# Performance work log

Hardware: AMD Instinct MI355X
Metric: run time of the kernel (lower is better)

Reference implementation:

```python
import jax, jax.numpy as jnp
import numpy as np

NORM_EPS = 1e-6
QK_SCALE = 1.0 / 128.0  # 1/d_head (muP)
ROTARY_BASE = 10000
INFTY_APPROX = 1e30

B, T, M, H, D = 2, 2048, 1024, 8, 128


def _rmsnorm(x, eps=NORM_EPS):
    # normalize over the last (head) dim; no learned gains (norm_gains=False)
    ms = jnp.mean(jnp.square(x), axis=-1, keepdims=True)
    return x / jnp.sqrt(ms + eps)


def _rope(x, base=ROTARY_BASE):
    # x: [b, h, t, d]; rotate (even-half, odd-half) pairs as in the source
    length, width = x.shape[-2], x.shape[-1]
    half = width // 2
    pos = jnp.arange(length, dtype=x.dtype)[:, None]            # [t, 1]
    freqs = jnp.power(jnp.asarray(base, x.dtype), -jnp.arange(half, dtype=x.dtype) / half)[None, :]
    rad = pos * freqs                                            # [t, half]
    cos = jnp.cos(rad)[None, None]
    sin = jnp.sin(rad)[None, None]
    even, odd = jnp.split(x, 2, axis=-1)
    return jnp.concatenate([even * cos - odd * sin, even * sin + odd * cos], axis=-1)


def setup_inputs() -> dict:
    key = jax.random.key(0)
    ks = jax.random.split(key, 5)
    std = M ** -0.5
    return {
        "x": jax.random.normal(ks[0], (B, T, M), jnp.float32),
        "wq": jax.random.normal(ks[1], (M, H, D), jnp.float32) * std,
        "wk": jax.random.normal(ks[2], (M, H, D), jnp.float32) * std,
        "wv": jax.random.normal(ks[3], (M, H, D), jnp.float32) * std,
        "wo": jax.random.normal(ks[4], (H, D, M), jnp.float32) * std,
    }


def reference(x, wq, wk, wv, wo):
    # projections: [b, h, t, d]
    q = jnp.einsum('bim,mhd->bhid', x, wq)
    k = jnp.einsum('bim,mhd->bhid', x, wk)
    v = jnp.einsum('bim,mhd->bhid', x, wv)
    # qk RMSNorm (norm_gains=False)
    q = _rmsnorm(q)
    k = _rmsnorm(k)
    # inline RoPE
    q = _rope(q)
    k = _rope(k)
    # scaled scores: mult applied to both q and k (mult^2 = qk_scale)
    mult = jnp.asarray(QK_SCALE ** 0.5, q.dtype)
    s = jnp.einsum('bhid,bhjd->bhij', q * mult, k * mult)
    # causal mask: subtract large constant where i < j
    t = s.shape[-1]
    mask = (jnp.arange(t)[:, None] < jnp.arange(t)[None, :]).astype(s.dtype)
    s = s - jnp.asarray(INFTY_APPROX, s.dtype) * mask[None, None]
    p = jax.nn.softmax(s, axis=-1)
    o = jnp.einsum('bhij,bhjd->bhid', p, v)
    return jnp.einsum('bhid,hdm->bim', o, wo)
```

## Files before the change

kernel.cpp:

```cpp
#include <hip/hip_runtime.h>
#include <hip/hip_bf16.h>
#include <math.h>

#define B_  2
#define T_  2048
#define M_  1024
#define H_  8
#define D_  128
#define NROW (B_ * T_)
#define HD  (H_ * D_)

#define NORM_EPS 1e-6f
#define QK_MULT  0.08838834764831845f
#define LN_BASE_64 0.14391156510f

typedef short bf16x8  __attribute__((ext_vector_type(8)));
typedef float f32x4   __attribute__((ext_vector_type(4)));
typedef float f32x16  __attribute__((ext_vector_type(16)));

static __device__ __forceinline__ unsigned short f2bf(float f) {
    union { __hip_bfloat16 h; unsigned short u; } cv;
    cv.h = __float2bfloat16(f);
    return cv.u;
}
static __device__ __forceinline__ float bf2f(unsigned short u) {
    union { unsigned short u; __hip_bfloat16 h; } cv;
    cv.u = u;
    return __bfloat162float(cv.h);
}
static __device__ __forceinline__ unsigned int pk2bf(float a, float b) {
    return ((unsigned int)f2bf(b) << 16) | f2bf(a);
}

static __device__ __forceinline__ void gload_lds16(const unsigned short* g,
                                                   unsigned short* l) {
    __builtin_amdgcn_global_load_lds(
        (const __attribute__((address_space(1))) void*)g,
        (__attribute__((address_space(3))) void*)l, 16, 0, 0);
}

__global__ __launch_bounds__(256) void prep(const float* __restrict__ x,
                                            const float* __restrict__ w0,
                                            const float* __restrict__ w1,
                                            const float* __restrict__ w2,
                                            const float* __restrict__ w3,
                                            unsigned short* __restrict__ xb,
                                            unsigned short* __restrict__ wqkvT,
                                            unsigned short* __restrict__ woT)
{
    __shared__ float t[32][33];
    const int z = blockIdx.z;
    if (z == 4) {
        const size_t base = ((size_t)blockIdx.y * 32 + blockIdx.x) * 4096;
        #pragma unroll
        for (int it = 0; it < 4; ++it) {
            const size_t i = base + it * 1024 + threadIdx.x * 4;
            const float4 v = *(const float4*)(x + i);
            ushort4 o;
            o.x = f2bf(v.x); o.y = f2bf(v.y); o.z = f2bf(v.z); o.w = f2bf(v.w);
            *(ushort4*)(xb + i) = o;
        }
        return;
    }
    const float* in = z == 0 ? w0 : (z == 1 ? w1 : (z == 2 ? w2 : w3));
    unsigned short* out = z < 3 ? (wqkvT + (size_t)z * 1024 * 1024) : woT;

    const int tx = threadIdx.x & 31;
    const int ty = threadIdx.x >> 5;
    const int n0 = blockIdx.x * 32;
    const int k0 = blockIdx.y * 32;
    #pragma unroll
    for (int r = 0; r < 4; ++r)
        t[ty + r * 8][tx] = in[(size_t)(k0 + ty + r * 8) * 1024 + n0 + tx];
    __syncthreads();
    #pragma unroll
    for (int r = 0; r < 4; ++r)
        out[(size_t)(n0 + ty + r * 8) * 1024 + k0 + tx] = f2bf(t[tx][ty + r * 8]);
}

template <int MODE>
__global__ __launch_bounds__(256) void gemm_bt(const unsigned short* __restrict__ A,
                                               const unsigned short* __restrict__ Bt,
                                               unsigned short* __restrict__ oq,
                                               unsigned short* __restrict__ ok,
                                               unsigned short* __restrict__ vt,
                                               float* __restrict__ cf)
{
    __shared__ __align__(16) unsigned short pool[128 * 132 + 512];
    unsigned short* As = pool;
    unsigned short* Bs = pool + 128 * 32;

    const int tid  = threadIdx.x;
    const int lane = tid & 63;
    const int w    = tid >> 6;
    const int g    = lane >> 4;
    const int lc   = lane & 15;
    const int wm   = w >> 1;
    const int wn   = w & 1;

    const int m0 = blockIdx.y * 128;
    const int n0 = blockIdx.x * 128;

    const unsigned short* aBase = A  + (size_t)m0 * 1024;
    const unsigned short* bBase = Bt + (size_t)n0 * 1024;

    f32x4 acc[4][4];
    #pragma unroll
    for (int i = 0; i < 4; ++i)
        #pragma unroll
        for (int j = 0; j < 4; ++j)
            acc[i][j] = (f32x4){0.f, 0.f, 0.f, 0.f};

    for (int kt = 0; kt < 32; ++kt) {
        const int k0 = kt * 32;
        #pragma unroll
        for (int it = 0; it < 2; ++it) {
            const int u  = tid + it * 256;
            const int r2 = u >> 2;
            const int s2 = u & 3;
            gload_lds16(aBase + (size_t)r2 * 1024 + k0 + s2 * 8, &As[u * 8]);
            gload_lds16(bBase + (size_t)r2 * 1024 + k0 + s2 * 8, &Bs[u * 8]);
        }
        __syncthreads();

        bf16x8 af[4], bfr[4];
        #pragma unroll
        for (int i = 0; i < 4; ++i)
            af[i] = *(const bf16x8*)&As[(wm * 64 + i * 16 + lc) * 32 + g * 8];
        #pragma unroll
        for (int j = 0; j < 4; ++j)
            bfr[j] = *(const bf16x8*)&Bs[(wn * 64 + j * 16 + lc) * 32 + g * 8];

        #pragma unroll
        for (int i = 0; i < 4; ++i)
            #pragma unroll
            for (int j = 0; j < 4; ++j)
                acc[i][j] = __builtin_amdgcn_mfma_f32_16x16x32_bf16(af[i], bfr[j], acc[i][j], 0, 0, 0);
        __syncthreads();
    }

    if (MODE == 0) {
        const int which = n0 >> 10;
        const int ncol0 = (n0 & 1023) + wn * 64;
        if (which < 2) {
            unsigned short* outp = which == 0 ? oq : ok;
            unsigned short* xbuf = pool;
            float* sqbuf = (float*)(pool + 128 * 132);

            float sq[4][4];
            #pragma unroll
            for (int i = 0; i < 4; ++i)
                #pragma unroll
                for (int r = 0; r < 4; ++r) {
                    float s = acc[i][0][r] * acc[i][0][r] + acc[i][1][r] * acc[i][1][r]
                            + acc[i][2][r] * acc[i][2][r] + acc[i][3][r] * acc[i][3][r];
                    #pragma unroll
                    for (int off = 1; off < 16; off <<= 1) s += __shfl_xor(s, off);
                    sq[i][r] = s;
                }
            if (lc == 0) {
                #pragma unroll
                for (int i = 0; i < 4; ++i)
                    #pragma unroll
                    for (int r = 0; r < 4; ++r)
                        sqbuf[wn * 128 + wm * 64 + i * 16 + g * 4 + r] = sq[i][r];
            }
            __syncthreads();

            #pragma unroll
            for (int i = 0; i < 4; ++i)
                #pragma unroll
                for (int r = 0; r < 4; ++r) {
                    const int row = wm * 64 + i * 16 + g * 4 + r;
                    const float tot = sqbuf[row] + sqbuf[128 + row];
                    const float rms = rsqrtf(tot * (1.0f / 128.0f) + NORM_EPS) * QK_MULT;
                    #pragma unroll
                    for (int j = 0; j < 4; ++j) {
                        acc[i][j][r] *= rms;
                        xbuf[row * 132 + wn * 64 + j * 16 + lc] = f2bf(acc[i][j][r]);
                    }
                }
            __syncthreads();

            float freq[4];
            #pragma unroll
            for (int j = 0; j < 4; ++j)
                freq[j] = __expf(-(float)(j * 16 + lc) * LN_BASE_64);
            #pragma unroll
            for (int i = 0; i < 4; ++i)
                #pragma unroll
                for (int r = 0; r < 4; ++r) {
                    const int row  = wm * 64 + i * 16 + g * 4 + r;
                    const int trow = m0 + row;
                    const float tpos = (float)(trow & (T_ - 1));
                    #pragma unroll
                    for (int j = 0; j < 4; ++j) {
                        float sn, cs;
                        __sincosf(tpos * freq[j], &sn, &cs);
                        const float own = acc[i][j][r];
                        const float par = bf2f(xbuf[row * 132 + ((wn ^ 1) * 64) + j * 16 + lc]);
                        const float outv = (wn == 0) ? (own * cs - par * sn)
                                                     : (par * sn + own * cs);
                        outp[(size_t)trow * 1024 + ncol0 + j * 16 + lc] = f2bf(outv);
                    }
                }
        } else {
            const int b2 = m0 >> 11;
            #pragma unroll
            for (int i = 0; i < 4; ++i) {
                const int t = (m0 & 2047) + wm * 64 + i * 16 + g * 4;
                #pragma unroll
                for (int j = 0; j < 4; ++j) {
                    const int nc = ncol0 + j * 16 + lc;
                    const int hh = nc >> 7, dd = nc & 127;
                    uint2 val;
                    val.x = pk2bf(acc[i][j][0], acc[i][j][1]);
                    val.y = pk2bf(acc[i][j][2], acc[i][j][3]);
                    *(uint2*)(vt + (((size_t)(b2 * 8 + hh) * 128 + dd) * T_ + t)) = val;
                }
            }
        }
    } else {
        #pragma unroll
        for (int i = 0; i < 4; ++i) {
            const int mrow = m0 + wm * 64 + i * 16 + g * 4;
            #pragma unroll
            for (int j = 0; j < 4; ++j) {
                const int nc = n0 + wn * 64 + j * 16 + lc;
                #pragma unroll
                for (int r = 0; r < 4; ++r)
                    cf[(size_t)(mrow + r) * 1024 + nc] = acc[i][j][r];
            }
        }
    }
}

__global__ __launch_bounds__(256) void flash_attn(const unsigned short* __restrict__ qb,
                                                  const unsigned short* __restrict__ kb,
                                                  const unsigned short* __restrict__ vt,
                                                  unsigned short* __restrict__ o)
{
    __shared__ __align__(16) unsigned short smem[2 * 64 * 128 + 2 * 128 * 64 + 128];
    unsigned short* KsB = smem;
    unsigned short* VsB = smem + 2 * 64 * 128;
    float* lscr = (float*)(smem + 2 * 64 * 128 + 2 * 128 * 64);
    float* scr  = (float*)smem;

    const int tid  = threadIdx.x;
    const int lane = tid & 63;
    const int w    = tid >> 6;
    const int wj   = w >> 1;
    const int wq2  = w & 1;
    const int qcol = lane & 31;
    const int hi   = lane >> 5;

    const int bh = blockIdx.x;
    const int h  = bh & (H_ - 1);
    const int b  = bh >> 3;
    const int yy = blockIdx.y;
    const int qt = (yy & 1) ? (31 - (yy >> 1)) : (yy >> 1);
    const int q0 = qt * 64;

    const size_t bhbase  = (size_t)b * T_ * HD + (size_t)h * 128;
    const size_t bhvbase = (size_t)bh * 128 * T_;

    int mI[4];
    size_t srcKoff[4], srcVoff[4];
    #pragma unroll
    for (int it = 0; it < 4; ++it) {
        const int m = (w * 4 + it) * 64 + lane;
        mI[it] = m;
        const int jK = m >> 4, cK = (m & 15) ^ (jK & 15);
        srcKoff[it] = (size_t)jK * 1024 + cK * 8;
        const int dV = m >> 3, cV = (m & 7) ^ (dV & 7);
        srcVoff[it] = (size_t)dV * T_ + cV * 8;
    }
    const unsigned short* kgb = kb + bhbase;
    const unsigned short* vgb = vt + bhvbase;

    bf16x8 qf[8];
    {
        const unsigned short* qp = qb + bhbase + (size_t)(q0 + wq2 * 32 + qcol) * 1024 + hi * 8;
        #pragma unroll
        for (int ks = 0; ks < 8; ++ks)
            qf[ks] = *(const bf16x8*)(qp + ks * 16);
    }

    float lsum = 0.f;
    f32x16 otacc[4];
    #pragma unroll
    for (int dch = 0; dch < 4; ++dch)
        #pragma unroll
        for (int r = 0; r < 16; ++r) otacc[dch][r] = 0.f;

    #pragma unroll
    for (int it = 0; it < 4; ++it) {
        gload_lds16(kgb + srcKoff[it], &KsB[mI[it] * 8]);
        gload_lds16(vgb + srcVoff[it], &VsB[mI[it] * 8]);
    }

    for (int jt = 0; jt <= qt; ++jt) {
        const int cur = jt & 1;
        unsigned short* Ks = KsB + cur * (64 * 128);
        unsigned short* Vs = VsB + cur * (128 * 64);
        __syncthreads();

        if (jt < qt) {
            const size_t j0n = (size_t)(jt + 1) * 64;
            unsigned short* Kn = KsB + (cur ^ 1) * (64 * 128);
            unsigned short* Vn = VsB + (cur ^ 1) * (128 * 64);
            #pragma unroll
            for (int it = 0; it < 4; ++it) {
                gload_lds16(kgb + j0n * 1024 + srcKoff[it], &Kn[mI[it] * 8]);
                gload_lds16(vgb + j0n + srcVoff[it], &Vn[mI[it] * 8]);
            }
        }

        const bool dead = (jt == qt) && (wj > wq2);
        if (!dead) {
            f32x16 sacc;
            #pragma unroll
            for (int r = 0; r < 16; ++r) sacc[r] = 0.f;
            const int jrow = wj * 32 + qcol;
            #pragma unroll
            for (int ks = 0; ks < 8; ++ks) {
                const int c = ks * 2 + hi;
                bf16x8 af = *(const bf16x8*)&Ks[(jrow * 16 + (c ^ (lane & 15))) * 8];
                sacc = __builtin_amdgcn_mfma_f32_32x32x16_bf16(af, qf[ks], sacc, 0, 0, 0);
            }

            if (jt == qt && wj == wq2) {
                #pragma unroll
                for (int r = 0; r < 16; ++r) {
                    const int jl = (r & 3) + 8 * (r >> 2) + 4 * hi;
                    if (qcol < jl) sacc[r] = -1e30f;
                }
            }

            unsigned int dw[8];
            #pragma unroll
            for (int m2 = 0; m2 < 8; ++m2) {
                const float p0 = __expf(sacc[2 * m2]);
                const float p1 = __expf(sacc[2 * m2 + 1]);
                lsum += p0 + p1;
                dw[m2] = pk2bf(p0, p1);
            }
            unsigned int ex[8];
            #pragma unroll
            for (int m2 = 0; m2 < 8; ++m2)
                ex[m2] = (unsigned int)__shfl_xor((int)dw[m2], 32);

            #pragma unroll
            for (int ks2 = 0; ks2 < 2; ++ks2) {
                union { unsigned int u[4]; bf16x8 v; } pf;
                pf.u[0] = hi ? ex[4 * ks2 + 2] : dw[4 * ks2 + 0];
                pf.u[1] = hi ? ex[4 * ks2 + 3] : dw[4 * ks2 + 1];
                pf.u[2] = hi ? dw[4 * ks2 + 2] : ex[4 * ks2 + 0];
                pf.u[3] = hi ? dw[4 * ks2 + 3] : ex[4 * ks2 + 1];
                #pragma unroll
                for (int dch = 0; dch < 4; ++dch) {
                    const int c = wj * 4 + ks2 * 2 + hi;
                    const int drow = dch * 32 + qcol;
                    bf16x8 af = *(const bf16x8*)&Vs[(drow * 8 + (c ^ (lane & 7))) * 8];
                    otacc[dch] = __builtin_amdgcn_mfma_f32_32x32x16_bf16(af, pf.v, otacc[dch], 0, 0, 0);
                }
            }
        }
    }

    lsum += __shfl_xor(lsum, 32);
    __syncthreads();

    if (wj == 1) {
        float* s0 = scr + (size_t)(wq2 * 32 + qcol) * 129;
        #pragma unroll
        for (int dch = 0; dch < 4; ++dch)
            #pragma unroll
            for (int r = 0; r < 16; ++r)
                s0[dch * 32 + (r & 3) + 8 * (r >> 2) + 4 * hi] = otacc[dch][r];
        if (hi == 0) lscr[wq2 * 32 + qcol] = lsum;
    }
    __syncthreads();
    if (wj == 0) {
        const float l = lsum + lscr[wq2 * 32 + qcol];
        const float inv = 1.0f / l;
        const float* s0 = scr + (size_t)(wq2 * 32 + qcol) * 129;
        unsigned short* op = o + bhbase + (size_t)(q0 + wq2 * 32 + qcol) * 1024;
        #pragma unroll
        for (int dch = 0; dch < 4; ++dch) {
            #pragma unroll
            for (int k4 = 0; k4 < 4; ++k4) {
                const int d0 = dch * 32 + 8 * k4 + 4 * hi;
                const float f0 = (otacc[dch][4 * k4 + 0] + s0[d0 + 0]) * inv;
                const float f1 = (otacc[dch][4 * k4 + 1] + s0[d0 + 1]) * inv;
                const float f2 = (otacc[dch][4 * k4 + 2] + s0[d0 + 2]) * inv;
                const float f3 = (otacc[dch][4 * k4 + 3] + s0[d0 + 3]) * inv;
                uint2 val;
                val.x = pk2bf(f0, f1);
                val.y = pk2bf(f2, f3);
                *(uint2*)(op + d0) = val;
            }
        }
    }
}

extern "C" void kernel_launch(void* const* d_in, const int* in_sizes, int n_in,
                              void* d_out, int out_size, void* d_ws, size_t ws_size,
                              hipStream_t stream)
{
    const float* x  = (const float*)d_in[0];
    const float* wq = (const float*)d_in[1];
    const float* wk = (const float*)d_in[2];
    const float* wv = (const float*)d_in[3];
    const float* wo = (const float*)d_in[4];
    float* out = (float*)d_out;

    const size_t SZ = (size_t)NROW * HD;
    unsigned short* qb    = (unsigned short*)d_ws;
    unsigned short* kb    = qb + SZ;
    unsigned short* vt    = kb + SZ;
    unsigned short* ob    = vt + SZ;
    unsigned short* xb    = ob + SZ;
    unsigned short* wqkvT = xb + SZ;
    unsigned short* woT   = wqkvT + 3 * 1024 * 1024;

    prep<<<dim3(32, 32, 5), 256, 0, stream>>>(x, wq, wk, wv, wo, xb, wqkvT, woT);

    gemm_bt<0><<<dim3(24, 32), 256, 0, stream>>>(xb, wqkvT, qb, kb, vt, nullptr);

    flash_attn<<<dim3(B_ * H_, 32), 256, 0, stream>>>(qb, kb, vt, ob);

    gemm_bt<1><<<dim3(8, 32), 256, 0, stream>>>(ob, woT, nullptr, nullptr, nullptr, out);
}
```

Before: 203.7 us.

## Split GEMM into QKV and output kernels with per-warp full-head tiles

The QKV GEMM now gives each warp 32 rows by all 128 columns, so one warp holds a whole head row. The RMSNorm sum and the RoPE pairing of the two halves then run in registers, with no LDS round trip or extra barriers. The output GEMM uses 128x64 tiles, doubling the block count to 512 for better CU occupancy. The trade-off is more B-fragment LDS reads per warp in the QKV kernel, and the output kernel now reads the A matrix twice as often overall.

```diff
diff --git a/kernel.cpp b/kernel.cpp
--- a/kernel.cpp
+++ b/kernel.cpp
@@ -78,17 +78,119 @@
         out[(size_t)(n0 + ty + r * 8) * 1024 + k0 + tx] = f2bf(t[tx][ty + r * 8]);
 }
 
-template <int MODE>
-__global__ __launch_bounds__(256) void gemm_bt(const unsigned short* __restrict__ A,
-                                               const unsigned short* __restrict__ Bt,
-                                               unsigned short* __restrict__ oq,
-                                               unsigned short* __restrict__ ok,
-                                               unsigned short* __restrict__ vt,
-                                               float* __restrict__ cf)
+__global__ __launch_bounds__(256) void gemm_qkv(const unsigned short* __restrict__ A,
+                                                const unsigned short* __restrict__ Bt,
+                                                unsigned short* __restrict__ oq,
+                                                unsigned short* __restrict__ ok,
+                                                unsigned short* __restrict__ vt)
 {
-    __shared__ __align__(16) unsigned short pool[128 * 132 + 512];
-    unsigned short* As = pool;
-    unsigned short* Bs = pool + 128 * 32;
+    __shared__ unsigned short As[128 * 32];
+    __shared__ unsigned short Bs[128 * 32];
+
+    const int tid  = threadIdx.x;
+    const int lane = tid & 63;
+    const int w    = tid >> 6;
+    const int g    = lane >> 4;
+    const int lc   = lane & 15;
+
+    const int m0 = blockIdx.y * 128;
+    const int n0 = blockIdx.x * 128;
+
+    const unsigned short* aBase = A  + (size_t)m0 * 1024;
+    const unsigned short* bBase = Bt + (size_t)n0 * 1024;
+
+    f32x4 acc[2][8];
+    #pragma unroll
+    for (int i = 0; i < 2; ++i)
+        #pragma unroll
+        for (int j = 0; j < 8; ++j)
+            acc[i][j] = (f32x4){0.f, 0.f, 0.f, 0.f};
+
+    for (int kt = 0; kt < 32; ++kt) {
+        const int k0 = kt * 32;
+        #pragma unroll
+        for (int it = 0; it < 2; ++it) {
+            const int u  = tid + it * 256;
+            const int r2 = u >> 2;
+            const int s2 = u & 3;
+            gload_lds16(aBase + (size_t)r2 * 1024 + k0 + s2 * 8, &As[u * 8]);
+            gload_lds16(bBase + (size_t)r2 * 1024 + k0 + s2 * 8, &Bs[u * 8]);
+        }
+        __syncthreads();
+
+        bf16x8 af[2], bfr[8];
+        #pragma unroll
+        for (int i = 0; i < 2; ++i)
+            af[i] = *(const bf16x8*)&As[(w * 32 + i * 16 + lc) * 32 + g * 8];
+        #pragma unroll
+        for (int j = 0; j < 8; ++j)
+            bfr[j] = *(const bf16x8*)&Bs[(j * 16 + lc) * 32 + g * 8];
+
+        #pragma unroll
+        for (int i = 0; i < 2; ++i)
+            #pragma unroll
+            for (int j = 0; j < 8; ++j)
+                acc[i][j] = __builtin_amdgcn_mfma_f32_16x16x32_bf16(af[i], bfr[j], acc[i][j], 0, 0, 0);
+        __syncthreads();
+    }
+
+    const int which = n0 >> 10;
+    const int ncol0 = n0 & 1023;
+    if (which < 2) {
+        unsigned short* outp = which == 0 ? oq : ok;
+        float freq[4];
+        #pragma unroll
+        for (int j = 0; j < 4; ++j)
+            freq[j] = __expf(-(float)(j * 16 + lc) * LN_BASE_64);
+
+        #pragma unroll
+        for (int i = 0; i < 2; ++i)
+            #pragma unroll
+            for (int r = 0; r < 4; ++r) {
+                float s = 0.f;
+                #pragma unroll
+                for (int j = 0; j < 8; ++j) s += acc[i][j][r] * acc[i][j][r];
+                #pragma unroll
+                for (int off = 1; off < 16; off <<= 1) s += __shfl_xor(s, off);
+                const float rms = rsqrtf(s * (1.0f / 128.0f) + NORM_EPS) * QK_MULT;
+
+                const int trow = m0 + w * 32 + i * 16 + g * 4 + r;
+                const float tpos = (float)(trow & (T_ - 1));
+                unsigned short* op = outp + (size_t)trow * 1024 + ncol0;
+                #pragma unroll
+                for (int j = 0; j < 4; ++j) {
+                    float sn, cs;
+                    __sincosf(tpos * freq[j], &sn, &cs);
+                    const float e = acc[i][j][r] * rms;
+                    const float o = acc[i][j + 4][r] * rms;
+                    op[j * 16 + lc]      = f2bf(e * cs - o * sn);
+                    op[j * 16 + lc + 64] = f2bf(e * sn + o * cs);
+                }
+            }
+    } else {
+        const int b2 = m0 >> 11;
+        const int hh = ncol0 >> 7;
+        #pragma unroll
+        for (int i = 0; i < 2; ++i) {
+            const int t = (m0 & 2047) + w * 32 + i * 16 + g * 4;
+            #pragma unroll
+            for (int j = 0; j < 8; ++j) {
+                const int dd = j * 16 + lc;
+                uint2 val;
+                val.x = pk2bf(acc[i][j][0], acc[i][j][1]);
+                val.y = pk2bf(acc[i][j][2], acc[i][j][3]);
+                *(uint2*)(vt + (((size_t)(b2 * 8 + hh) * 128 + dd) * T_ + t)) = val;
+            }
+        }
+    }
+}
+
+__global__ __launch_bounds__(256) void gemm_out(const unsigned short* __restrict__ A,
+                                                const unsigned short* __restrict__ Bt,
+                                                float* __restrict__ cf)
+{
+    __shared__ unsigned short As[128 * 32];
+    __shared__ unsigned short Bs[64 * 32];
 
     const int tid  = threadIdx.x;
     const int lane = tid & 63;
@@ -99,16 +201,16 @@
     const int wn   = w & 1;
 
     const int m0 = blockIdx.y * 128;
-    const int n0 = blockIdx.x * 128;
+    const int n0 = blockIdx.x * 64;
 
     const unsigned short* aBase = A  + (size_t)m0 * 1024;
     const unsigned short* bBase = Bt + (size_t)n0 * 1024;
 
-    f32x4 acc[4][4];
+    f32x4 acc[4][2];
     #pragma unroll
     for (int i = 0; i < 4; ++i)
         #pragma unroll
-        for (int j = 0; j < 4; ++j)
+        for (int j = 0; j < 2; ++j)
             acc[i][j] = (f32x4){0.f, 0.f, 0.f, 0.f};
 
     for (int kt = 0; kt < 32; ++kt) {
@@ -116,121 +218,36 @@
         #pragma unroll
         for (int it = 0; it < 2; ++it) {
             const int u  = tid + it * 256;
-            const int r2 = u >> 2;
-            const int s2 = u & 3;
-            gload_lds16(aBase + (size_t)r2 * 1024 + k0 + s2 * 8, &As[u * 8]);
-            gload_lds16(bBase + (size_t)r2 * 1024 + k0 + s2 * 8, &Bs[u * 8]);
-        }
+            gload_lds16(aBase + (size_t)(u >> 2) * 1024 + k0 + (u & 3) * 8, &As[u * 8]);
+        }
+        gload_lds16(bBase + (size_t)(tid >> 2) * 1024 + k0 + (tid & 3) * 8, &Bs[tid * 8]);
         __syncthreads();
 
-        bf16x8 af[4], bfr[4];
+        bf16x8 af[4], bfr[2];
         #pragma unroll
         for (int i = 0; i < 4; ++i)
             af[i] = *(const bf16x8*)&As[(wm * 64 + i * 16 + lc) * 32 + g * 8];
         #pragma unroll
-        for (int j = 0; j < 4; ++j)
-            bfr[j] = *(const bf16x8*)&Bs[(wn * 64 + j * 16 + lc) * 32 + g * 8];
+        for (int j = 0; j < 2; ++j)
+            bfr[j] = *(const bf16x8*)&Bs[(wn * 32 + j * 16 + lc) * 32 + g * 8];
 
         #pragma unroll
         for (int i = 0; i < 4; ++i)
             #pragma unroll
-            for (int j = 0; j < 4; ++j)
+            for (int j = 0; j < 2; ++j)
                 acc[i][j] = __builtin_amdgcn_mfma_f32_16x16x32_bf16(af[i], bfr[j], acc[i][j], 0, 0, 0);
         __syncthreads();
     }
 
-    if (MODE == 0) {
-        const int which = n0 >> 10;
-        const int ncol0 = (n0 & 1023) + wn * 64;
-        if (which < 2) {
-            unsigned short* outp = which == 0 ? oq : ok;
-            unsigned short* xbuf = pool;
-            float* sqbuf = (float*)(pool + 128 * 132);
-
-            float sq[4][4];
-            #pragma unroll
-            for (int i = 0; i < 4; ++i)
-                #pragma unroll
-                for (int r = 0; r < 4; ++r) {
-                    float s = acc[i][0][r] * acc[i][0][r] + acc[i][1][r] * acc[i][1][r]
-                            + acc[i][2][r] * acc[i][2][r] + acc[i][3][r] * acc[i][3][r];
-                    #pragma unroll
-                    for (int off = 1; off < 16; off <<= 1) s += __shfl_xor(s, off);
-                    sq[i][r] = s;
-                }
-            if (lc == 0) {
-                #pragma unroll
-                for (int i = 0; i < 4; ++i)
-                    #pragma unroll
-                    for (int r = 0; r < 4; ++r)
-                        sqbuf[wn * 128 + wm * 64 + i * 16 + g * 4 + r] = sq[i][r];
-            }
-            __syncthreads();
-
-            #pragma unroll
-            for (int i = 0; i < 4; ++i)
-                #pragma unroll
-                for (int r = 0; r < 4; ++r) {
-                    const int row = wm * 64 + i * 16 + g * 4 + r;
-                    const float tot = sqbuf[row] + sqbuf[128 + row];
-                    const float rms = rsqrtf(tot * (1.0f / 128.0f) + NORM_EPS) * QK_MULT;
-                    #pragma unroll
-                    for (int j = 0; j < 4; ++j) {
-                        acc[i][j][r] *= rms;
-                        xbuf[row * 132 + wn * 64 + j * 16 + lc] = f2bf(acc[i][j][r]);
-                    }
-                }
-            __syncthreads();
-
-            float freq[4];
-            #pragma unroll
-            for (int j = 0; j < 4; ++j)
-                freq[j] = __expf(-(float)(j * 16 + lc) * LN_BASE_64);
-            #pragma unroll
-            for (int i = 0; i < 4; ++i)
-                #pragma unroll
-                for (int r = 0; r < 4; ++r) {
-                    const int row  = wm * 64 + i * 16 + g * 4 + r;
-                    const int trow = m0 + row;
-                    const float tpos = (float)(trow & (T_ - 1));
-                    #pragma unroll
-                    for (int j = 0; j < 4; ++j) {
-                        float sn, cs;
-                        __sincosf(tpos * freq[j], &sn, &cs);
-                        const float own = acc[i][j][r];
-                        const float par = bf2f(xbuf[row * 132 + ((wn ^ 1) * 64) + j * 16 + lc]);
-                        const float outv = (wn == 0) ? (own * cs - par * sn)
-                                                     : (par * sn + own * cs);
-                        outp[(size_t)trow * 1024 + ncol0 + j * 16 + lc] = f2bf(outv);
-                    }
-                }
-        } else {
-            const int b2 = m0 >> 11;
-            #pragma unroll
-            for (int i = 0; i < 4; ++i) {
-                const int t = (m0 & 2047) + wm * 64 + i * 16 + g * 4;
-                #pragma unroll
-                for (int j = 0; j < 4; ++j) {
-                    const int nc = ncol0 + j * 16 + lc;
-                    const int hh = nc >> 7, dd = nc & 127;
-                    uint2 val;
-                    val.x = pk2bf(acc[i][j][0], acc[i][j][1]);
-                    val.y = pk2bf(acc[i][j][2], acc[i][j][3]);
-                    *(uint2*)(vt + (((size_t)(b2 * 8 + hh) * 128 + dd) * T_ + t)) = val;
-                }
-            }
-        }
-    } else {
-        #pragma unroll
-        for (int i = 0; i < 4; ++i) {
-            const int mrow = m0 + wm * 64 + i * 16 + g * 4;
-            #pragma unroll
-            for (int j = 0; j < 4; ++j) {
-                const int nc = n0 + wn * 64 + j * 16 + lc;
-                #pragma unroll
-                for (int r = 0; r < 4; ++r)
-                    cf[(size_t)(mrow + r) * 1024 + nc] = acc[i][j][r];
-            }
+    #pragma unroll
+    for (int i = 0; i < 4; ++i) {
+        const int mrow = m0 + wm * 64 + i * 16 + g * 4;
+        #pragma unroll
+        for (int j = 0; j < 2; ++j) {
+            const int nc = n0 + wn * 32 + j * 16 + lc;
+            #pragma unroll
+            for (int r = 0; r < 4; ++r)
+                cf[(size_t)(mrow + r) * 1024 + nc] = acc[i][j][r];
         }
     }
 }
@@ -426,9 +443,9 @@
 
     prep<<<dim3(32, 32, 5), 256, 0, stream>>>(x, wq, wk, wv, wo, xb, wqkvT, woT);
 
-    gemm_bt<0><<<dim3(24, 32), 256, 0, stream>>>(xb, wqkvT, qb, kb, vt, nullptr);
+    gemm_qkv<<<dim3(24, 32), 256, 0, stream>>>(xb, wqkvT, qb, kb, vt);
 
     flash_attn<<<dim3(B_ * H_, 32), 256, 0, stream>>>(qb, kb, vt, ob);
 
-    gemm_bt<1><<<dim3(8, 32), 256, 0, stream>>>(ob, woT, nullptr, nullptr, nullptr, out);
-}
+    gemm_out<<<dim3(16, 32), 256, 0, stream>>>(ob, woT, out);
+}
```

After: 196.2 us. -3.7%, faster.
